# Kernel optimization log

Hardware: AMD Instinct MI355X
Metric: run time of the kernel (lower is better)

## Reference

```python
import jax, jax.numpy as jnp
import numpy as np

B, L, IN_DIM, OUT_DIM, N_BRANCH = 16, 1024, 300, 100, 60

def setup_inputs() -> dict:
    key = jax.random.key(0)
    ks = jax.random.split(key, 7)
    s = 0.05  # weight init scale
    return {
        "x": jax.random.normal(ks[0], (B, L, IN_DIM), dtype=jnp.float32),
        "W2": jax.random.normal(ks[1], (N_BRANCH, OUT_DIM, IN_DIM, 2), dtype=jnp.float32) * s,
        "b2": jax.random.normal(ks[2], (N_BRANCH, OUT_DIM), dtype=jnp.float32) * s,
        "W3": jax.random.normal(ks[3], (N_BRANCH, OUT_DIM, IN_DIM, 3), dtype=jnp.float32) * s,
        "b3": jax.random.normal(ks[4], (N_BRANCH, OUT_DIM), dtype=jnp.float32) * s,
        "W4": jax.random.normal(ks[5], (N_BRANCH, OUT_DIM, IN_DIM, 4), dtype=jnp.float32) * s,
        "b4": jax.random.normal(ks[6], (N_BRANCH, OUT_DIM), dtype=jnp.float32) * s,
    }

def _branch_group(xc, W, b):
    # xc: [B, C, L]; W: [n, o, c, k]; b: [n, o]
    # Batch all n same-kernel-size branches into ONE conv with n*o output channels.
    n, o, c, k = W.shape
    Wf = W.reshape(n * o, c, k)
    y = jax.lax.conv_general_dilated(
        xc, Wf, window_strides=(1,), padding="VALID",
        dimension_numbers=("NCH", "OIH", "NCH"))  # [B, n*o, L-k+1]
    y = jax.nn.relu(y + b.reshape(n * o)[None, :, None])
    y = jnp.max(y, axis=-1)                      # AdaptiveMaxPool1d(1): [B, n*o]
    # concat dim=2 in torch stacks branches along the length axis -> [B, o, n]
    return jnp.transpose(y.reshape(xc.shape[0], n, o), (0, 2, 1))

def reference(x, W2, b2, W3, b3, W4, b4):
    xc = jnp.transpose(x, (0, 2, 1))  # [B, in_dim, L]
    out = jnp.concatenate([
        _branch_group(xc, W2, b2),
        _branch_group(xc, W3, b3),
        _branch_group(xc, W4, b4),
    ], axis=2)                        # [B, out_dim, 180]
    # nn.Dropout(0.5) is identity in eval mode; omitted for the reference baseline.
    return out
```

## Files before the change

kernel.cpp:

```cpp
#include <hip/hip_runtime.h>
#include <cstdint>
#include <cstddef>

typedef unsigned short u16;
typedef unsigned int   u32;
typedef __attribute__((ext_vector_type(8))) short bf16x8;
typedef __attribute__((ext_vector_type(4))) float f32x4;

#define NB   16
#define LL   1024
#define CIN  300
#define CINP 320
#define XPBP (LL*CINP)
#define XELP (NB*XPBP)
#define NCH  6000
#define NCHP 6144
#define ODIM 100

#define BM 256
#define BN 256
#define BK 64

__device__ __forceinline__ u16 f2bf(float f) {
  union { float f; u32 u; } v; v.f = f;
  return (u16)((v.u + 0x7FFFu + ((v.u >> 16) & 1u)) >> 16);
}

typedef __attribute__((address_space(1))) const unsigned int gu32;
typedef __attribute__((address_space(3))) unsigned int lu32;
__device__ __forceinline__ void gload_lds16(const void* g, void* l) {
  __builtin_amdgcn_global_load_lds((gu32*)g, (lu32*)l, 16, 0, 0);
}

#define BAR() asm volatile("s_barrier" ::: "memory")

__global__ void cvt_x_kernel(const float* __restrict__ x, u16* __restrict__ xb) {
  int i8 = (blockIdx.x * 256 + threadIdx.x) * 8;
  int row = i8 / CINP;
  int col = i8 - row * CINP;
  const float* src = x + (size_t)row * CIN + col;
  u16 e[8];
  if (col + 8 <= CIN) {
    float4 a = *(const float4*)src;
    float4 b = *(const float4*)(src + 4);
    e[0]=f2bf(a.x); e[1]=f2bf(a.y); e[2]=f2bf(a.z); e[3]=f2bf(a.w);
    e[4]=f2bf(b.x); e[5]=f2bf(b.y); e[6]=f2bf(b.z); e[7]=f2bf(b.w);
  } else {
    #pragma unroll
    for (int j = 0; j < 8; j++)
      e[j] = (col + j < CIN) ? f2bf(src[j]) : (u16)0;
  }
  uint4 o;
  o.x = (u32)e[0] | ((u32)e[1] << 16);
  o.y = (u32)e[2] | ((u32)e[3] << 16);
  o.z = (u32)e[4] | ((u32)e[5] << 16);
  o.w = (u32)e[6] | ((u32)e[7] << 16);
  *(uint4*)(xb + i8) = o;
}

__global__ void repack_w_kernel(const float* __restrict__ W2, const float* __restrict__ W3,
                                const float* __restrict__ W4, u16* __restrict__ wb) {
  int g = blockIdx.y;
  int kk = g + 2;
  int Kp = kk * CINP;
  int woff = (g == 0) ? 0 : (g == 1) ? NCHP*640 : NCHP*(640+960);
  const float* W = (g == 0) ? W2 : (g == 1) ? W3 : W4;
  int no = blockIdx.x;
  u16* dst = wb + (size_t)woff + (size_t)no * Kp;
  const float* src = W + (size_t)no * (CIN * kk);
  for (int kp = threadIdx.x; kp < Kp; kp += 256) {
    int j = kp / CINP, c = kp - j * CINP;
    u16 v = 0;
    if (no < NCH && c < CIN) v = f2bf(src[c * kk + j]);
    dst[kp] = v;
  }
}

__global__ __launch_bounds__(512, 1)
void gemm_max_kernel(const u16* __restrict__ xb, const u16* __restrict__ wb,
                     const float* __restrict__ b2v, const float* __restrict__ b3v,
                     const float* __restrict__ b4v, float* __restrict__ out) {
  const int id    = blockIdx.x;
  const int g     = 2 - (id / 384);
  const int id2   = id % 384;
  const int b     = id2 / 24;
  const int chblk = id2 % 24;
  const int Kp    = (g + 2) * CINP;
  const int nks   = Kp >> 6;
  const int woff  = (g == 0) ? 0 : (g == 1) ? NCHP*640 : NCHP*(640+960);
  const int Lt    = LL - (g + 2) + 1;

  __shared__ __align__(16) u16 smem[4 * 16384];
  u16* A0s = smem;
  u16* B0s = smem + 16384;
  u16* A1s = smem + 32768;
  u16* B1s = smem + 49152;

  const int tid  = threadIdx.x;
  const int lane = tid & 63;
  const int w    = tid >> 6;
  const int wr   = w >> 2;
  const int wc   = w & 3;

  const u16* __restrict__ xrow = xb + (size_t)b * XPBP;
  const u16* __restrict__ Wg   = wb + (size_t)woff + (size_t)chblk * BN * Kp;

  auto STAGE = [&](const u16* src, int stride, u16* buf, int half) {
    #pragma unroll
    for (int i = 0; i < 2; i++) {
      int c = i * 512 + w * 64 + lane;
      int row128 = c >> 3;
      int colb = ((c & 7) * 16) ^ ((row128 & 7) << 4);
      gload_lds16(src + (size_t)(half * 128 + row128) * stride + (colb >> 1),
                  buf + half * 8192 + i * 4096 + w * 512);
    }
  };

  auto FR = [&](const u16* buf, int grp, int k) -> bf16x8 {
    int row  = grp * 16 + (lane & 15);
    int colb = (k * 64 + ((lane >> 4) << 4)) ^ ((lane & 7) << 4);
    return *(const bf16x8*)(buf + row * 64 + (colb >> 1));
  };

  f32x4 acc[8][4];
  #pragma unroll
  for (int mi = 0; mi < 8; mi++)
    #pragma unroll
    for (int ni = 0; ni < 4; ni++)
      acc[mi][ni] = (f32x4){0.f, 0.f, 0.f, 0.f};

  bf16x8 afr[4][2];
  bf16x8 bfr[2][2][2];
  float rmax[4] = { -1e30f, -1e30f, -1e30f, -1e30f };

  auto FOLD = [&](int ttf) {
    #pragma unroll
    for (int mi = 0; mi < 8; mi++) {
      int tb = ttf * 256 + (mi * 2 + wr) * 16 + ((lane >> 4) << 2);
      #pragma unroll
      for (int r = 0; r < 4; r++) {
        bool ok = (tb + r) < Lt;
        #pragma unroll
        for (int ni = 0; ni < 4; ni++)
          if (ok) rmax[ni] = fmaxf(rmax[ni], acc[mi][ni][r]);
      }
      #pragma unroll
      for (int ni = 0; ni < 4; ni++)
        acc[mi][ni] = (f32x4){0.f, 0.f, 0.f, 0.f};
    }
  };

#define PHASE(CA, CB, MHC, NH, RA, RB, STG, VM) do {                          \
    if (RA) {                                                                 \
      _Pragma("unroll")                                                       \
      for (int a2 = 0; a2 < 4; a2++) {                                        \
        _Pragma("unroll")                                                     \
        for (int k2 = 0; k2 < 2; k2++)                                        \
          afr[a2][k2] = FR(CA, ((MHC)*4 + a2) * 2 + wr, k2);                  \
      }                                                                       \
    }                                                                         \
    if (RB) {                                                                 \
      _Pragma("unroll")                                                       \
      for (int b2 = 0; b2 < 2; b2++) {                                        \
        _Pragma("unroll")                                                     \
        for (int k2 = 0; k2 < 2; k2++)                                        \
          bfr[NH][b2][k2] = FR(CB, ((NH)*2 + b2) * 4 + wc, k2);               \
      }                                                                       \
    }                                                                         \
    STG;                                                                      \
    BAR();                                                                    \
    __builtin_amdgcn_s_setprio(1);                                            \
    _Pragma("unroll")                                                         \
    for (int a2 = 0; a2 < 4; a2++)                                            \
      _Pragma("unroll")                                                       \
      for (int b2 = 0; b2 < 2; b2++)                                          \
        _Pragma("unroll")                                                     \
        for (int k2 = 0; k2 < 2; k2++)                                        \
          acc[(MHC)*4 + a2][(NH)*2 + b2] =                                    \
            __builtin_amdgcn_mfma_f32_16x16x32_bf16(afr[a2][k2],              \
              bfr[NH][b2][k2], acc[(MHC)*4 + a2][(NH)*2 + b2], 0, 0, 0);      \
    __builtin_amdgcn_s_setprio(0);                                            \
    VM;                                                                       \
    BAR();                                                                    \
  } while (0)

  const int NT = 4 * nks;
  int tt = 0, ks = 0;

  STAGE(xrow, CINP, A0s, 0);
  STAGE(Wg,   Kp,   B0s, 0);
  STAGE(Wg,   Kp,   B0s, 1);
  STAGE(xrow, CINP, A0s, 1);
  asm volatile("s_waitcnt vmcnt(4)" ::: "memory");
  BAR();

  for (int s = 0; s < NT - 1; s++) {
    int ks2 = ks + 1, tt2 = tt;
    if (ks2 == nks) { ks2 = 0; tt2++; }
    const u16* sA = xrow + (size_t)tt2 * (256 * CINP) + ks2 * 64;
    const u16* sB = Wg + ks2 * 64;
    u16* cA = (s & 1) ? A1s : A0s;
    u16* cB = (s & 1) ? B1s : B0s;
    u16* nA = (s & 1) ? A0s : A1s;
    u16* nB = (s & 1) ? B0s : B1s;

    PHASE(cA, cB, 0, 0, 1, 1, STAGE(sA, CINP, nA, 0),
          asm volatile("s_waitcnt vmcnt(4)" ::: "memory"));
    PHASE(cA, cB, 0, 1, 0, 1, STAGE(sB, Kp,   nB, 0),
          asm volatile("s_waitcnt vmcnt(4)" ::: "memory"));
    PHASE(cA, cB, 1, 0, 1, 0, STAGE(sB, Kp,   nB, 1),
          ((void)0));
    PHASE(cA, cB, 1, 1, 0, 0, STAGE(sA, CINP, nA, 1),
          asm volatile("s_waitcnt vmcnt(4) lgkmcnt(0)" ::: "memory"));

    if (++ks == nks) { FOLD(tt); ks = 0; tt++; }
  }

  {
    u16* cA = A1s;
    u16* cB = B1s;
    PHASE(cA, cB, 0, 0, 1, 1, ((void)0),
          asm volatile("s_waitcnt vmcnt(2)" ::: "memory"));
    PHASE(cA, cB, 0, 1, 0, 1, ((void)0),
          asm volatile("s_waitcnt vmcnt(0)" ::: "memory"));
    PHASE(cA, cB, 1, 0, 1, 0, ((void)0), ((void)0));
    PHASE(cA, cB, 1, 1, 0, 0, ((void)0),
          asm volatile("s_waitcnt lgkmcnt(0)" ::: "memory"));
    FOLD(tt);
  }
#undef PHASE

  float cv[4];
  #pragma unroll
  for (int ni = 0; ni < 4; ni++) {
    float v = rmax[ni];
    v = fmaxf(v, __shfl_xor(v, 16));
    v = fmaxf(v, __shfl_xor(v, 32));
    cv[ni] = v;
  }
  __syncthreads();
  float* red = (float*)smem;
  if (lane < 16) {
    #pragma unroll
    for (int ni = 0; ni < 4; ni++)
      red[wr * 256 + (ni * 4 + wc) * 16 + lane] = cv[ni];
  }
  __syncthreads();
  const float* bias = (g == 0) ? b2v : (g == 1) ? b3v : b4v;
  if (tid < 256) {
    float v = fmaxf(red[tid], red[256 + tid]);
    int ch = chblk * BN + tid;
    if (ch < NCH) {
      int n = ch / ODIM, o = ch - n * ODIM;
      out[b * (ODIM * 180) + o * 180 + g * 60 + n] = fmaxf(v + bias[ch], 0.f);
    }
  }
}

extern "C" void kernel_launch(void* const* d_in, const int* in_sizes, int n_in,
                              void* d_out, int out_size, void* d_ws, size_t ws_size,
                              hipStream_t stream) {
  const float* x  = (const float*)d_in[0];
  const float* W2 = (const float*)d_in[1];
  const float* b2 = (const float*)d_in[2];
  const float* W3 = (const float*)d_in[3];
  const float* b3 = (const float*)d_in[4];
  const float* W4 = (const float*)d_in[5];
  const float* b4 = (const float*)d_in[6];
  float* out = (float*)d_out;

  u16* xb = (u16*)d_ws;
  u16* wb = xb + XELP;

  cvt_x_kernel<<<XELP / (256 * 8), 256, 0, stream>>>(x, xb);
  repack_w_kernel<<<dim3(NCHP, 3), 256, 0, stream>>>(W2, W3, W4, wb);
  gemm_max_kernel<<<dim3(1152), 512, 0, stream>>>(xb, wb, b2, b3, b4, out);
}
```

Measured before the change: 531.9 us.

## Software-pipeline LDS fragment reads ahead of MFMA quadrants with double-buffered A registers

Restructures the GEMM main loop so that LDS fragment reads for the next quadrant (and the next k-step's first A/B fragments) are issued while the current quadrant's MFMAs run. A second A-fragment register set is added so reads can overlap compute. Wait counts are relaxed from vmcnt(4) to vmcnt(2) and the barrier placement is changed. This raises register pressure and depends on the new barrier and waitcnt ordering being correct for the shared LDS buffers.

```diff
diff --git a/kernel.cpp b/kernel.cpp
--- a/kernel.cpp
+++ b/kernel.cpp
@@ -33,6 +33,8 @@
 }
 
 #define BAR() asm volatile("s_barrier" ::: "memory")
+#define VM2  asm volatile("s_waitcnt vmcnt(2)" ::: "memory")
+#define VM0  asm volatile("s_waitcnt vmcnt(0)" ::: "memory")
 
 __global__ void cvt_x_kernel(const float* __restrict__ x, u16* __restrict__ xb) {
   int i8 = (blockIdx.x * 256 + threadIdx.x) * 8;
@@ -129,7 +131,8 @@
     for (int ni = 0; ni < 4; ni++)
       acc[mi][ni] = (f32x4){0.f, 0.f, 0.f, 0.f};
 
-  bf16x8 afr[4][2];
+  bf16x8 afrA[4][2];
+  bf16x8 afrB[4][2];
   bf16x8 bfr[2][2][2];
   float rmax[4] = { -1e30f, -1e30f, -1e30f, -1e30f };
 
@@ -150,25 +153,25 @@
     }
   };
 
-#define PHASE(CA, CB, MHC, NH, RA, RB, STG, VM) do {                          \
-    if (RA) {                                                                 \
+#define READ_A(DST, BUF, MH) do {                                             \
+    _Pragma("unroll")                                                         \
+    for (int a2 = 0; a2 < 4; a2++) {                                          \
       _Pragma("unroll")                                                       \
-      for (int a2 = 0; a2 < 4; a2++) {                                        \
-        _Pragma("unroll")                                                     \
-        for (int k2 = 0; k2 < 2; k2++)                                        \
-          afr[a2][k2] = FR(CA, ((MHC)*4 + a2) * 2 + wr, k2);                  \
-      }                                                                       \
+      for (int k2 = 0; k2 < 2; k2++)                                          \
+        DST[a2][k2] = FR(BUF, ((MH)*4 + a2) * 2 + wr, k2);                    \
     }                                                                         \
-    if (RB) {                                                                 \
+  } while (0)
+
+#define READ_B(NH, BUF) do {                                                  \
+    _Pragma("unroll")                                                         \
+    for (int b2 = 0; b2 < 2; b2++) {                                          \
       _Pragma("unroll")                                                       \
-      for (int b2 = 0; b2 < 2; b2++) {                                        \
-        _Pragma("unroll")                                                     \
-        for (int k2 = 0; k2 < 2; k2++)                                        \
-          bfr[NH][b2][k2] = FR(CB, ((NH)*2 + b2) * 4 + wc, k2);               \
-      }                                                                       \
+      for (int k2 = 0; k2 < 2; k2++)                                          \
+        bfr[NH][b2][k2] = FR(BUF, ((NH)*2 + b2) * 4 + wc, k2);                \
     }                                                                         \
-    STG;                                                                      \
-    BAR();                                                                    \
+  } while (0)
+
+#define MFMAQ(MH, NH, A) do {                                                 \
     __builtin_amdgcn_s_setprio(1);                                            \
     _Pragma("unroll")                                                         \
     for (int a2 = 0; a2 < 4; a2++)                                            \
@@ -176,12 +179,10 @@
       for (int b2 = 0; b2 < 2; b2++)                                          \
         _Pragma("unroll")                                                     \
         for (int k2 = 0; k2 < 2; k2++)                                        \
-          acc[(MHC)*4 + a2][(NH)*2 + b2] =                                    \
-            __builtin_amdgcn_mfma_f32_16x16x32_bf16(afr[a2][k2],              \
-              bfr[NH][b2][k2], acc[(MHC)*4 + a2][(NH)*2 + b2], 0, 0, 0);      \
+          acc[(MH)*4 + a2][(NH)*2 + b2] =                                     \
+            __builtin_amdgcn_mfma_f32_16x16x32_bf16(A[a2][k2],                \
+              bfr[NH][b2][k2], acc[(MH)*4 + a2][(NH)*2 + b2], 0, 0, 0);       \
     __builtin_amdgcn_s_setprio(0);                                            \
-    VM;                                                                       \
-    BAR();                                                                    \
   } while (0)
 
   const int NT = 4 * nks;
@@ -191,8 +192,10 @@
   STAGE(Wg,   Kp,   B0s, 0);
   STAGE(Wg,   Kp,   B0s, 1);
   STAGE(xrow, CINP, A0s, 1);
-  asm volatile("s_waitcnt vmcnt(4)" ::: "memory");
+  VM2;
   BAR();
+  READ_A(afrA, A0s, 0);
+  READ_B(0, B0s);
 
   for (int s = 0; s < NT - 1; s++) {
     int ks2 = ks + 1, tt2 = tt;
@@ -204,31 +207,47 @@
     u16* nA = (s & 1) ? A0s : A1s;
     u16* nB = (s & 1) ? B0s : B1s;
 
-    PHASE(cA, cB, 0, 0, 1, 1, STAGE(sA, CINP, nA, 0),
-          asm volatile("s_waitcnt vmcnt(4)" ::: "memory"));
-    PHASE(cA, cB, 0, 1, 0, 1, STAGE(sB, Kp,   nB, 0),
-          asm volatile("s_waitcnt vmcnt(4)" ::: "memory"));
-    PHASE(cA, cB, 1, 0, 1, 0, STAGE(sB, Kp,   nB, 1),
-          ((void)0));
-    PHASE(cA, cB, 1, 1, 0, 0, STAGE(sA, CINP, nA, 1),
-          asm volatile("s_waitcnt vmcnt(4) lgkmcnt(0)" ::: "memory"));
+    STAGE(sA, CINP, nA, 0);
+    BAR();
+    MFMAQ(0, 0, afrA);
+    VM2;
+    READ_B(1, cB);
+    BAR();
+    STAGE(sB, Kp, nB, 0);
+    BAR();
+    MFMAQ(0, 1, afrA);
+    READ_A(afrB, cA, 1);
+    BAR();
+    STAGE(sB, Kp, nB, 1);
+    BAR();
+    MFMAQ(1, 0, afrB);
+    VM2;
+    BAR();
+    STAGE(sA, CINP, nA, 1);
+    BAR();
+    MFMAQ(1, 1, afrB);
+    VM2;
+    READ_A(afrA, nA, 0);
+    READ_B(0, nB);
+    BAR();
 
     if (++ks == nks) { FOLD(tt); ks = 0; tt++; }
   }
 
   {
-    u16* cA = A1s;
-    u16* cB = B1s;
-    PHASE(cA, cB, 0, 0, 1, 1, ((void)0),
-          asm volatile("s_waitcnt vmcnt(2)" ::: "memory"));
-    PHASE(cA, cB, 0, 1, 0, 1, ((void)0),
-          asm volatile("s_waitcnt vmcnt(0)" ::: "memory"));
-    PHASE(cA, cB, 1, 0, 1, 0, ((void)0), ((void)0));
-    PHASE(cA, cB, 1, 1, 0, 0, ((void)0),
-          asm volatile("s_waitcnt lgkmcnt(0)" ::: "memory"));
+    MFMAQ(0, 0, afrA);
+    VM0;
+    READ_B(1, B1s);
+    BAR();
+    MFMAQ(0, 1, afrA);
+    READ_A(afrB, A1s, 1);
+    MFMAQ(1, 0, afrB);
+    MFMAQ(1, 1, afrB);
     FOLD(tt);
   }
-#undef PHASE
+#undef READ_A
+#undef READ_B
+#undef MFMAQ
 
   float cv[4];
   #pragma unroll
```

New measurement: 537.5 us. Within noise of the previous version (+1.0%).
